# Kernel optimization log

Measured on AMD Instinct MI355X. Metric: run time of the kernel, lower is better.

## Reference

```python
import jax, jax.numpy as jnp
import numpy as np

B, D, C, E, H = 65536, 512, 101, 8, 256


def setup_inputs() -> dict:
    key = jax.random.key(0)
    ks = jax.random.split(key, 7)
    s_d = 1.0 / np.sqrt(D)
    s_h = 1.0 / np.sqrt(H)
    return {
        "x": jax.random.normal(ks[0], (B, D), dtype=jnp.float32),
        "W1": jax.random.uniform(ks[1], (E, D, H), jnp.float32, -s_d, s_d),  # expert layer1
        "b1": jax.random.uniform(ks[2], (E, H), jnp.float32, -s_d, s_d),
        "W2": jax.random.uniform(ks[3], (E, H, C), jnp.float32, -s_h, s_h),  # expert layer2
        "b2": jax.random.uniform(ks[4], (E, C), jnp.float32, -s_h, s_h),
        "Wg": jax.random.uniform(ks[5], (D, E), jnp.float32, -s_d, s_d),     # gate
        "bg": jax.random.uniform(ks[6], (E,), jnp.float32, -s_d, s_d),
    }


def reference(x, W1, b1, W2, b2, Wg, bg):
    # gate: softmax over experts
    gates = jax.nn.softmax(x @ Wg + bg, axis=1)                 # [B, E]
    # all experts: batched two-layer MLP
    h = jax.nn.relu(jnp.einsum("bd,edh->beh", x, W1) + b1)      # [B, E, H]
    eo = jnp.einsum("beh,ehc->bec", h, W2) + b2                 # [B, E, C]
    # gate-weighted sum over experts
    return jnp.einsum("be,bec->bc", gates, eo)                  # [B, C]
```

## Files before the change

kernel.cpp:

```cpp
#include <hip/hip_runtime.h>


typedef __attribute__((ext_vector_type(8))) short short8x;
typedef __attribute__((ext_vector_type(4))) float float4x;

#define C_DIM 101

__device__ __forceinline__ unsigned short f2bf(float f) {
  unsigned int u = __builtin_bit_cast(unsigned int, f);
  u += 0x7fffu + ((u >> 16) & 1u);
  return (unsigned short)(u >> 16);
}

__global__ void conv_weights(const float* __restrict__ W1, const float* __restrict__ Wg,
                             const float* __restrict__ W2,
                             unsigned short* __restrict__ W1bf,
                             unsigned short* __restrict__ W2bf) {
  if (blockIdx.x < 516) {
    int s = blockIdx.x * blockDim.x + threadIdx.x;
    int l = s & 63;
    int frag = s >> 6;
    int kf = frag & 15;
    int ntile = frag >> 4;
    int n = (ntile << 4) | (l & 15);
    int k = (kf << 5) | ((l >> 4) << 3);
    short8x v;
#pragma unroll
    for (int j = 0; j < 8; ++j) {
      int kk = k + j;
      float f;
      if (n < 2048)      f = W1[((size_t)(n >> 8) * 512 + kk) * 256 + (n & 255)];
      else if (n < 2056) f = Wg[(size_t)kk * 8 + (n - 2048)];
      else               f = 0.f;
      v[j] = (short)f2bf(f);
    }
    *(short8x*)(W1bf + (size_t)s * 8) = v;
  } else {
    int s = (blockIdx.x - 516) * blockDim.x + threadIdx.x;
    int l = s & 63;
    int frag = s >> 6;
    int kf = frag & 63;
    int ntile = frag >> 6;
    int c = (ntile << 4) | (l & 15);
    int k = (kf << 5) | ((l >> 4) << 3);
    short8x v;
#pragma unroll
    for (int j = 0; j < 8; ++j) {
      int kk = k + j;
      float f = (c < C_DIM) ? W2[((size_t)(kk >> 8) * 256 + (kk & 255)) * C_DIM + c] : 0.f;
      v[j] = (short)f2bf(f);
    }
    *(short8x*)(W2bf + (size_t)s * 8) = v;
  }
}

__global__ __launch_bounds__(512, 2) void moe_main(
    const float* __restrict__ x, const float* __restrict__ b1,
    const float* __restrict__ b2, const float* __restrict__ bg,
    const unsigned short* __restrict__ W1bf, const unsigned short* __restrict__ W2bf,
    float* __restrict__ out) {
  __shared__ unsigned short xA[64 * 512];
  __shared__ unsigned short hA[64 * 512];
  __shared__ float gt[8 * 64];
  float* graw = (float*)hA;

  const int tid = threadIdx.x;
  const int w = tid >> 6;
  const int l = tid & 63;
  const int quad = l >> 4;
  const int p = l & 15;
  const int r0 = blockIdx.x * 64;

#pragma unroll
  for (int it = 0; it < 8; ++it) {
    int g = tid + it * 512;
    int m = g >> 6;
    int k0 = (g & 63) << 3;
    const float* src = x + (size_t)(r0 + m) * 512 + k0;
    float4 f0 = *(const float4*)src;
    float4 f1 = *(const float4*)(src + 4);
    short8x v;
    v[0] = (short)f2bf(f0.x); v[1] = (short)f2bf(f0.y);
    v[2] = (short)f2bf(f0.z); v[3] = (short)f2bf(f0.w);
    v[4] = (short)f2bf(f1.x); v[5] = (short)f2bf(f1.y);
    v[6] = (short)f2bf(f1.z); v[7] = (short)f2bf(f1.w);
    int mt = m >> 4;
    int kfrag = k0 >> 5;
    int lane = (((k0 >> 3) & 3) << 4) | (m & 15);
    *(short8x*)&xA[(size_t)(((mt << 4) | kfrag) * 64 + lane) * 8] = v;
  }
  __syncthreads();

  if (w < 4) {
    float4x acc = {0.f, 0.f, 0.f, 0.f};
#pragma unroll 2
    for (int kf = 0; kf < 16; ++kf) {
      short8x a = *(const short8x*)&xA[(size_t)((w * 16 + kf) * 64 + l) * 8];
      short8x b = *(const short8x*)(W1bf + ((size_t)(128 * 16 + kf) * 512 + l * 8));
      acc = __builtin_amdgcn_mfma_f32_16x16x32_bf16(a, b, acc, 0, 0, 0);
    }
    if (p < 8) {
      float bgv = bg[p];
#pragma unroll
      for (int r = 0; r < 4; ++r)
        graw[(w * 16 + quad * 4 + r) * 8 + p] = acc[r] + bgv;
    }
  }
  __syncthreads();
  if (tid < 64) {
    float v[8], mx = -1e30f;
#pragma unroll
    for (int e = 0; e < 8; ++e) { v[e] = graw[tid * 8 + e]; mx = fmaxf(mx, v[e]); }
    float s = 0.f;
#pragma unroll
    for (int e = 0; e < 8; ++e) { v[e] = expf(v[e] - mx); s += v[e]; }
    float inv = 1.f / s;
#pragma unroll
    for (int e = 0; e < 8; ++e) gt[e * 64 + tid] = v[e] * inv;
  }
  __syncthreads();

  float4x zero = {0.f, 0.f, 0.f, 0.f};
  float4x acc2[4];
  acc2[0] = zero; acc2[1] = zero; acc2[2] = zero; acc2[3] = zero;

  for (int it = 0; it < 4; ++it) {
#pragma unroll
    for (int eo = 0; eo < 2; ++eo) {
      const int e = it * 2 + eo;
      float4x acc1[4][2];
#pragma unroll
      for (int mt = 0; mt < 4; ++mt) { acc1[mt][0] = zero; acc1[mt][1] = zero; }

      const unsigned short* __restrict__ bp =
          W1bf + ((size_t)(e * 16 + w * 2) * 16) * 512 + (size_t)l * 8;
      short8x aC0 = *(const short8x*)&xA[(size_t)((0 * 16 + 0) * 64 + l) * 8];
      short8x aC1 = *(const short8x*)&xA[(size_t)((1 * 16 + 0) * 64 + l) * 8];
      short8x aC2 = *(const short8x*)&xA[(size_t)((2 * 16 + 0) * 64 + l) * 8];
      short8x aC3 = *(const short8x*)&xA[(size_t)((3 * 16 + 0) * 64 + l) * 8];
      short8x bC0 = *(const short8x*)(bp);
      short8x bC1 = *(const short8x*)(bp + 8192);
#pragma unroll
      for (int kf = 0; kf < 16; ++kf) {
        short8x aN0, aN1, aN2, aN3, bN0, bN1;
        if (kf < 15) {
          bN0 = *(const short8x*)(bp + (kf + 1) * 512);
          bN1 = *(const short8x*)(bp + 8192 + (kf + 1) * 512);
          aN0 = *(const short8x*)&xA[(size_t)((0 * 16 + kf + 1) * 64 + l) * 8];
          aN1 = *(const short8x*)&xA[(size_t)((1 * 16 + kf + 1) * 64 + l) * 8];
          aN2 = *(const short8x*)&xA[(size_t)((2 * 16 + kf + 1) * 64 + l) * 8];
          aN3 = *(const short8x*)&xA[(size_t)((3 * 16 + kf + 1) * 64 + l) * 8];
        }
        acc1[0][0] = __builtin_amdgcn_mfma_f32_16x16x32_bf16(aC0, bC0, acc1[0][0], 0, 0, 0);
        acc1[1][0] = __builtin_amdgcn_mfma_f32_16x16x32_bf16(aC1, bC0, acc1[1][0], 0, 0, 0);
        acc1[2][0] = __builtin_amdgcn_mfma_f32_16x16x32_bf16(aC2, bC0, acc1[2][0], 0, 0, 0);
        acc1[3][0] = __builtin_amdgcn_mfma_f32_16x16x32_bf16(aC3, bC0, acc1[3][0], 0, 0, 0);
        acc1[0][1] = __builtin_amdgcn_mfma_f32_16x16x32_bf16(aC0, bC1, acc1[0][1], 0, 0, 0);
        acc1[1][1] = __builtin_amdgcn_mfma_f32_16x16x32_bf16(aC1, bC1, acc1[1][1], 0, 0, 0);
        acc1[2][1] = __builtin_amdgcn_mfma_f32_16x16x32_bf16(aC2, bC1, acc1[2][1], 0, 0, 0);
        acc1[3][1] = __builtin_amdgcn_mfma_f32_16x16x32_bf16(aC3, bC1, acc1[3][1], 0, 0, 0);
        if (kf < 15) {
          aC0 = aN0; aC1 = aN1; aC2 = aN2; aC3 = aN3;
          bC0 = bN0; bC1 = bN1;
        }
      }

      if (eo == 0) __syncthreads();

      float4x gv0 = *(const float4x*)&gt[e * 64 + 0  + quad * 4];
      float4x gv1 = *(const float4x*)&gt[e * 64 + 16 + quad * 4];
      float4x gv2 = *(const float4x*)&gt[e * 64 + 32 + quad * 4];
      float4x gv3 = *(const float4x*)&gt[e * 64 + 48 + quad * 4];
#pragma unroll
      for (int nc = 0; nc < 2; ++nc) {
        int cw = w * 32 + nc * 16 + p;
        float b1v = b1[e * 256 + cw];
        int jj = p & 7;
        int ldbase = ((nc * 2 + (p >> 3)) << 4);
#pragma unroll
        for (int mt = 0; mt < 4; ++mt) {
          float4x gv = (mt == 0) ? gv0 : (mt == 1) ? gv1 : (mt == 2) ? gv2 : gv3;
#pragma unroll
          for (int r = 0; r < 4; ++r) {
            float hv = fmaxf(acc1[mt][nc][r] + b1v, 0.f) * gv[r];
            hA[(size_t)((eo * 32 + w * 4 + mt) * 512) + (ldbase + quad * 4 + r) * 8 + jj] =
                f2bf(hv);
          }
        }
      }
    }
    __syncthreads();

    if (w < 7) {
      const unsigned short* __restrict__ bp2 =
          W2bf + ((size_t)(w * 64 + it * 16)) * 512 + (size_t)l * 8;
      short8x b2C = *(const short8x*)(bp2);
      short8x a2C0 = *(const short8x*)&hA[(size_t)((0 * 4 + 0) * 64 + l) * 8];
      short8x a2C1 = *(const short8x*)&hA[(size_t)((0 * 4 + 1) * 64 + l) * 8];
      short8x a2C2 = *(const short8x*)&hA[(size_t)((0 * 4 + 2) * 64 + l) * 8];
      short8x a2C3 = *(const short8x*)&hA[(size_t)((0 * 4 + 3) * 64 + l) * 8];
#pragma unroll
      for (int s = 0; s < 16; ++s) {
        short8x b2N, a2N0, a2N1, a2N2, a2N3;
        if (s < 15) {
          b2N = *(const short8x*)(bp2 + (size_t)(s + 1) * 512);
          a2N0 = *(const short8x*)&hA[(size_t)(((s + 1) * 4 + 0) * 64 + l) * 8];
          a2N1 = *(const short8x*)&hA[(size_t)(((s + 1) * 4 + 1) * 64 + l) * 8];
          a2N2 = *(const short8x*)&hA[(size_t)(((s + 1) * 4 + 2) * 64 + l) * 8];
          a2N3 = *(const short8x*)&hA[(size_t)(((s + 1) * 4 + 3) * 64 + l) * 8];
        }
        acc2[0] = __builtin_amdgcn_mfma_f32_16x16x32_bf16(a2C0, b2C, acc2[0], 0, 0, 0);
        acc2[1] = __builtin_amdgcn_mfma_f32_16x16x32_bf16(a2C1, b2C, acc2[1], 0, 0, 0);
        acc2[2] = __builtin_amdgcn_mfma_f32_16x16x32_bf16(a2C2, b2C, acc2[2], 0, 0, 0);
        acc2[3] = __builtin_amdgcn_mfma_f32_16x16x32_bf16(a2C3, b2C, acc2[3], 0, 0, 0);
        if (s < 15) {
          a2C0 = a2N0; a2C1 = a2N1; a2C2 = a2N2; a2C3 = a2N3;
          b2C = b2N;
        }
      }
    }
  }

  if (w < 7) {
    int c = w * 16 + p;
    if (c < C_DIM) {
#pragma unroll
      for (int mt = 0; mt < 4; ++mt) {
#pragma unroll
        for (int r = 0; r < 4; ++r) {
          int row = mt * 16 + quad * 4 + r;
          float bias = 0.f;
#pragma unroll
          for (int e = 0; e < 8; ++e) bias += gt[e * 64 + row] * b2[e * C_DIM + c];
          out[(size_t)(r0 + row) * C_DIM + c] = acc2[mt][r] + bias;
        }
      }
    }
  }
}

extern "C" void kernel_launch(void* const* d_in, const int* in_sizes, int n_in,
                              void* d_out, int out_size, void* d_ws, size_t ws_size,
                              hipStream_t stream) {
  const float* x  = (const float*)d_in[0];
  const float* W1 = (const float*)d_in[1];
  const float* b1 = (const float*)d_in[2];
  const float* W2 = (const float*)d_in[3];
  const float* b2 = (const float*)d_in[4];
  const float* Wg = (const float*)d_in[5];
  const float* bg = (const float*)d_in[6];
  float* out = (float*)d_out;

  unsigned short* W1bf = (unsigned short*)d_ws;
  unsigned short* W2bf = (unsigned short*)((char*)d_ws + (size_t)129 * 16 * 512 * 2);

  conv_weights<<<644, 256, 0, stream>>>(W1, Wg, W2, W1bf, W2bf);
  moe_main<<<1024, 512, 0, stream>>>(x, b1, b2, bg, W1bf, W2bf, out);
}
```

Baseline: 377.3 us.

## Prefetch W1 fragments into registers across experts with split-half double buffering

Replaces the one-step-ahead register prefetch of W1 global loads with a two-half scheme. Each half holds 16 B fragments per thread. The first half of the next expert's W1 fragments is issued while the second half of the current expert's MFMAs runs, so global load latency is hidden behind more compute. The A operand from LDS is now loaded on demand instead of being prefetched. The change holds many more live vector registers, which risks spills or lower occupancy.

Result: no change. 377.3 us (-0.0%).

```diff
diff --git a/kernel.cpp b/kernel.cpp
--- a/kernel.cpp
+++ b/kernel.cpp
@@ -124,6 +124,17 @@
   float4x acc2[4];
   acc2[0] = zero; acc2[1] = zero; acc2[2] = zero; acc2[3] = zero;
 
+  short8x bfA[2][8], bfB[2][8];
+  {
+    const unsigned short* __restrict__ bp0 =
+        W1bf + ((size_t)(0 * 16 + w * 2) * 16) * 512 + (size_t)l * 8;
+#pragma unroll
+    for (int nc = 0; nc < 2; ++nc)
+#pragma unroll
+      for (int kf = 0; kf < 8; ++kf)
+        bfA[nc][kf] = *(const short8x*)(bp0 + (nc * 16 + kf) * 512);
+  }
+
   for (int it = 0; it < 4; ++it) {
 #pragma unroll
     for (int eo = 0; eo < 2; ++eo) {
@@ -134,35 +145,52 @@
 
       const unsigned short* __restrict__ bp =
           W1bf + ((size_t)(e * 16 + w * 2) * 16) * 512 + (size_t)l * 8;
-      short8x aC0 = *(const short8x*)&xA[(size_t)((0 * 16 + 0) * 64 + l) * 8];
-      short8x aC1 = *(const short8x*)&xA[(size_t)((1 * 16 + 0) * 64 + l) * 8];
-      short8x aC2 = *(const short8x*)&xA[(size_t)((2 * 16 + 0) * 64 + l) * 8];
-      short8x aC3 = *(const short8x*)&xA[(size_t)((3 * 16 + 0) * 64 + l) * 8];
-      short8x bC0 = *(const short8x*)(bp);
-      short8x bC1 = *(const short8x*)(bp + 8192);
-#pragma unroll
-      for (int kf = 0; kf < 16; ++kf) {
-        short8x aN0, aN1, aN2, aN3, bN0, bN1;
-        if (kf < 15) {
-          bN0 = *(const short8x*)(bp + (kf + 1) * 512);
-          bN1 = *(const short8x*)(bp + 8192 + (kf + 1) * 512);
-          aN0 = *(const short8x*)&xA[(size_t)((0 * 16 + kf + 1) * 64 + l) * 8];
-          aN1 = *(const short8x*)&xA[(size_t)((1 * 16 + kf + 1) * 64 + l) * 8];
-          aN2 = *(const short8x*)&xA[(size_t)((2 * 16 + kf + 1) * 64 + l) * 8];
-          aN3 = *(const short8x*)&xA[(size_t)((3 * 16 + kf + 1) * 64 + l) * 8];
-        }
-        acc1[0][0] = __builtin_amdgcn_mfma_f32_16x16x32_bf16(aC0, bC0, acc1[0][0], 0, 0, 0);
-        acc1[1][0] = __builtin_amdgcn_mfma_f32_16x16x32_bf16(aC1, bC0, acc1[1][0], 0, 0, 0);
-        acc1[2][0] = __builtin_amdgcn_mfma_f32_16x16x32_bf16(aC2, bC0, acc1[2][0], 0, 0, 0);
-        acc1[3][0] = __builtin_amdgcn_mfma_f32_16x16x32_bf16(aC3, bC0, acc1[3][0], 0, 0, 0);
-        acc1[0][1] = __builtin_amdgcn_mfma_f32_16x16x32_bf16(aC0, bC1, acc1[0][1], 0, 0, 0);
-        acc1[1][1] = __builtin_amdgcn_mfma_f32_16x16x32_bf16(aC1, bC1, acc1[1][1], 0, 0, 0);
-        acc1[2][1] = __builtin_amdgcn_mfma_f32_16x16x32_bf16(aC2, bC1, acc1[2][1], 0, 0, 0);
-        acc1[3][1] = __builtin_amdgcn_mfma_f32_16x16x32_bf16(aC3, bC1, acc1[3][1], 0, 0, 0);
-        if (kf < 15) {
-          aC0 = aN0; aC1 = aN1; aC2 = aN2; aC3 = aN3;
-          bC0 = bN0; bC1 = bN1;
-        }
+#pragma unroll
+      for (int nc = 0; nc < 2; ++nc)
+#pragma unroll
+        for (int kf = 0; kf < 8; ++kf)
+          bfB[nc][kf] = *(const short8x*)(bp + (nc * 16 + 8 + kf) * 512);
+
+#pragma unroll
+      for (int kf = 0; kf < 8; ++kf) {
+        short8x a0 = *(const short8x*)&xA[(size_t)((0 * 16 + kf) * 64 + l) * 8];
+        short8x a1 = *(const short8x*)&xA[(size_t)((1 * 16 + kf) * 64 + l) * 8];
+        short8x a2 = *(const short8x*)&xA[(size_t)((2 * 16 + kf) * 64 + l) * 8];
+        short8x a3 = *(const short8x*)&xA[(size_t)((3 * 16 + kf) * 64 + l) * 8];
+        acc1[0][0] = __builtin_amdgcn_mfma_f32_16x16x32_bf16(a0, bfA[0][kf], acc1[0][0], 0, 0, 0);
+        acc1[1][0] = __builtin_amdgcn_mfma_f32_16x16x32_bf16(a1, bfA[0][kf], acc1[1][0], 0, 0, 0);
+        acc1[2][0] = __builtin_amdgcn_mfma_f32_16x16x32_bf16(a2, bfA[0][kf], acc1[2][0], 0, 0, 0);
+        acc1[3][0] = __builtin_amdgcn_mfma_f32_16x16x32_bf16(a3, bfA[0][kf], acc1[3][0], 0, 0, 0);
+        acc1[0][1] = __builtin_amdgcn_mfma_f32_16x16x32_bf16(a0, bfA[1][kf], acc1[0][1], 0, 0, 0);
+        acc1[1][1] = __builtin_amdgcn_mfma_f32_16x16x32_bf16(a1, bfA[1][kf], acc1[1][1], 0, 0, 0);
+        acc1[2][1] = __builtin_amdgcn_mfma_f32_16x16x32_bf16(a2, bfA[1][kf], acc1[2][1], 0, 0, 0);
+        acc1[3][1] = __builtin_amdgcn_mfma_f32_16x16x32_bf16(a3, bfA[1][kf], acc1[3][1], 0, 0, 0);
+      }
+
+      if (e < 7) {
+        const unsigned short* __restrict__ bpn =
+            W1bf + ((size_t)((e + 1) * 16 + w * 2) * 16) * 512 + (size_t)l * 8;
+#pragma unroll
+        for (int nc = 0; nc < 2; ++nc)
+#pragma unroll
+          for (int kf = 0; kf < 8; ++kf)
+            bfA[nc][kf] = *(const short8x*)(bpn + (nc * 16 + kf) * 512);
+      }
+
+#pragma unroll
+      for (int kf = 0; kf < 8; ++kf) {
+        short8x a0 = *(const short8x*)&xA[(size_t)((0 * 16 + 8 + kf) * 64 + l) * 8];
+        short8x a1 = *(const short8x*)&xA[(size_t)((1 * 16 + 8 + kf) * 64 + l) * 8];
+        short8x a2 = *(const short8x*)&xA[(size_t)((2 * 16 + 8 + kf) * 64 + l) * 8];
+        short8x a3 = *(const short8x*)&xA[(size_t)((3 * 16 + 8 + kf) * 64 + l) * 8];
+        acc1[0][0] = __builtin_amdgcn_mfma_f32_16x16x32_bf16(a0, bfB[0][kf], acc1[0][0], 0, 0, 0);
+        acc1[1][0] = __builtin_amdgcn_mfma_f32_16x16x32_bf16(a1, bfB[0][kf], acc1[1][0], 0, 0, 0);
+        acc1[2][0] = __builtin_amdgcn_mfma_f32_16x16x32_bf16(a2, bfB[0][kf], acc1[2][0], 0, 0, 0);
+        acc1[3][0] = __builtin_amdgcn_mfma_f32_16x16x32_bf16(a3, bfB[0][kf], acc1[3][0], 0, 0, 0);
+        acc1[0][1] = __builtin_amdgcn_mfma_f32_16x16x32_bf16(a0, bfB[1][kf], acc1[0][1], 0, 0, 0);
+        acc1[1][1] = __builtin_amdgcn_mfma_f32_16x16x32_bf16(a1, bfB[1][kf], acc1[1][1], 0, 0, 0);
+        acc1[2][1] = __builtin_amdgcn_mfma_f32_16x16x32_bf16(a2, bfB[1][kf], acc1[2][1], 0, 0, 0);
+        acc1[3][1] = __builtin_amdgcn_mfma_f32_16x16x32_bf16(a3, bfB[1][kf], acc1[3][1], 0, 0, 0);
       }
 
       if (eo == 0) __syncthreads();
```
